# Performance work log

Hardware: AMD Instinct MI355X
Metric: run time of the kernel (lower is better)

Reference implementation:

```python
import jax, jax.numpy as jnp
import numpy as np

SOS_TOKEN = 0


def setup_inputs() -> dict:
    key = jax.random.key(0)
    ks = jax.random.split(key, 16)
    B, S, T, H, V = 64, 64, 32, 512, 32000
    s = 1.0 / np.sqrt(H)
    inp = {
        "encoder_outputs": jax.random.normal(ks[0], (B, S, H), jnp.float32),
        "encoder_hidden": jax.random.normal(ks[1], (1, B, H), jnp.float32),
        "target_tensor": jax.random.randint(ks[2], (B, T), 0, V),
        "emb": jax.random.normal(ks[3], (V, H), jnp.float32),
        "Wa": jax.random.uniform(ks[4], (H, H), jnp.float32, -s, s),
        "ba": jnp.zeros((H,), jnp.float32),
        "Ua": jax.random.uniform(ks[5], (H, H), jnp.float32, -s, s),
        "bu": jnp.zeros((H,), jnp.float32),
        "va": jax.random.uniform(ks[6], (H, 1), jnp.float32, -s, s),
        "bv": jnp.zeros((1,), jnp.float32),
        "w_ih": jax.random.uniform(ks[7], (3 * H, 2 * H), jnp.float32, -s, s),
        "b_ih": jax.random.uniform(ks[8], (3 * H,), jnp.float32, -s, s),
        "w_hh": jax.random.uniform(ks[9], (3 * H, H), jnp.float32, -s, s),
        "b_hh": jax.random.uniform(ks[10], (3 * H,), jnp.float32, -s, s),
        "Wo": jax.random.uniform(ks[11], (V, H), jnp.float32, -s, s),
        "bo": jax.random.uniform(ks[12], (V,), jnp.float32, -s, s),
    }
    return inp


def _gru_cell(x, h, w_ih, b_ih, w_hh, b_hh):
    # x: [B, 2H], h: [B, H] -- PyTorch nn.GRU gate math
    H = h.shape[-1]
    gi = x @ w_ih.T + b_ih            # [B, 3H]
    gh = h @ w_hh.T + b_hh            # [B, 3H]
    i_r, i_z, i_n = gi[:, :H], gi[:, H:2 * H], gi[:, 2 * H:]
    h_r, h_z, h_n = gh[:, :H], gh[:, H:2 * H], gh[:, 2 * H:]
    r = jax.nn.sigmoid(i_r + h_r)
    z = jax.nn.sigmoid(i_z + h_z)
    n = jnp.tanh(i_n + r * h_n)
    return (1.0 - z) * n + z * h


def reference(encoder_outputs, encoder_hidden, target_tensor,
              emb, Wa, ba, Ua, bu, va, bv,
              w_ih, b_ih, w_hh, b_hh, Wo, bo):
    B, S, H = encoder_outputs.shape
    T = target_tensor.shape[1]
    # Teacher forcing: step t input is SOS for t=0 else target[:, t-1]
    sos = jnp.full((B, 1), SOS_TOKEN, dtype=target_tensor.dtype)
    input_ids = jnp.concatenate([sos, target_tensor[:, :-1]], axis=1)  # [B, T]
    embedded = emb[input_ids]  # [B, T, H]  (dropout is identity in eval)

    # Precompute key projection once (invariant across steps)
    Ua_keys = encoder_outputs @ Ua.T + bu  # [B, S, H]

    def step(h, x_emb):
        # Bahdanau additive attention: query = hidden state
        scores = jnp.tanh(h[:, None, :] @ Wa.T + ba + Ua_keys) @ va + bv  # [B, S, 1]
        scores = scores[..., 0]                                           # [B, S]
        attn = jax.nn.softmax(scores, axis=-1)
        context = jnp.einsum('bs,bsh->bh', attn, encoder_outputs)
        x = jnp.concatenate([x_emb, context], axis=-1)                    # [B, 2H]
        h_new = _gru_cell(x, h, w_ih, b_ih, w_hh, b_hh)
        logits = h_new @ Wo.T + bo                                        # [B, V]
        return h_new, (logits, attn)

    h0 = encoder_hidden[0]  # [B, H]
    h_final, (logits_t, attn_t) = jax.lax.scan(step, h0, jnp.swapaxes(embedded, 0, 1))
    logits = jnp.swapaxes(logits_t, 0, 1)        # [B, T, V]
    attentions = jnp.swapaxes(attn_t, 0, 1)      # [B, T, S]
    log_probs = jax.nn.log_softmax(logits, axis=-1)
    decoder_hidden = h_final[None]               # [1, B, H]
    return (log_probs, decoder_hidden, attentions)
```

## Files before the change

### kernel.cpp

```cpp
#include <hip/hip_runtime.h>

typedef unsigned short u16;
typedef __bf16 bf16x8 __attribute__((ext_vector_type(8)));
typedef float f32x4 __attribute__((ext_vector_type(4)));

#define Bsz 64
#define Ssz 64
#define Tsz 32
#define Hsz 512
#define Vsz 32000
#define NCONV 160
#define NTOT 256

static __device__ inline u16 f2bf(float f) {
    union { float f; unsigned u; } v; v.f = f;
    unsigned u = v.u;
    unsigned r = (u + 0x7FFFu + ((u >> 16) & 1u)) >> 16;
    return (u16)r;
}
static __device__ inline float bf2f(u16 v) {
    union { unsigned u; float f; } x; x.u = ((unsigned)v) << 16; return x.f;
}
static __device__ inline float tanh_fast(float x) {
    float e = __expf(2.f * x);
    return 1.f - 2.f / (e + 1.f);
}
static __device__ inline void st_u32(unsigned* p, unsigned v) {
    __hip_atomic_store(p, v, __ATOMIC_RELAXED, __HIP_MEMORY_SCOPE_AGENT);
}
static __device__ inline unsigned ld_u32(const unsigned* p) {
    return __hip_atomic_load(p, __ATOMIC_RELAXED, __HIP_MEMORY_SCOPE_AGENT);
}

#define GLOAD_LDS16(g, l) \
    __builtin_amdgcn_global_load_lds((const __attribute__((address_space(1))) void*)(g), \
                                     (__attribute__((address_space(3))) void*)(l), 16, 0, 0)

__global__ void prep_kernel(const float* __restrict__ enc, const float* __restrict__ Ua,
                            const float* __restrict__ Wa, const float* __restrict__ wih,
                            const float* __restrict__ whh, const float* __restrict__ ehid,
                            const int* __restrict__ target, const float* __restrict__ emb,
                            u16* __restrict__ encbf, u16* __restrict__ Uabf,
                            u16* __restrict__ Wabf, u16* __restrict__ wihbf,
                            u16* __restrict__ whhbf, u16* __restrict__ h0bf,
                            u16* __restrict__ xbuf) {
    const int n0 = 2097152, n1 = 262144, n2 = 262144, n3 = 1572864, n4 = 786432, n5 = 32768;
    const int n6 = Tsz * Bsz * Hsz;
    const int total = n0 + n1 + n2 + n3 + n4 + n5 + n6;
    for (int i = blockIdx.x * blockDim.x + threadIdx.x; i < total; i += gridDim.x * blockDim.x) {
        int j = i;
        if (j < n0) { encbf[j] = f2bf(enc[j]); continue; } j -= n0;
        if (j < n1) { Uabf[j] = f2bf(Ua[j]); continue; } j -= n1;
        if (j < n2) { Wabf[j] = f2bf(Wa[j]); continue; } j -= n2;
        if (j < n3) { wihbf[j] = f2bf(wih[j]); continue; } j -= n3;
        if (j < n4) { whhbf[j] = f2bf(whh[j]); continue; } j -= n4;
        if (j < n5) { h0bf[j] = f2bf(ehid[j]); continue; } j -= n5;
        {
            int t = j / (Bsz * Hsz);
            int rem = j % (Bsz * Hsz);
            int b = rem / Hsz, k = rem % Hsz;
            int id = (t == 0) ? 0 : target[b * Tsz + (t - 1)];
            xbuf[((size_t)t * Bsz + b) * 1024 + k] = f2bf(emb[(size_t)id * Hsz + k]);
        }
    }
}

__global__ __launch_bounds__(256) void gemm_bt(const u16* __restrict__ A, const u16* __restrict__ Bw,
                                               const float* __restrict__ bias, float* __restrict__ out,
                                               int M, int N, int K) {
    __shared__ __align__(16) u16 As[128 * 32];
    __shared__ __align__(16) u16 Bs[128 * 32];
    int m0 = blockIdx.x * 128, n0 = blockIdx.y * 128;
    int tid = threadIdx.x, lane = tid & 63, wid = tid >> 6;
    int wm = wid & 1, wn = wid >> 1;
    f32x4 acc[4][4] = {};
    for (int k0 = 0; k0 < K; k0 += 32) {
        int e0 = wid * 64 + lane;
        int e1 = e0 + 256;
        GLOAD_LDS16(&A[(size_t)(m0 + (e0 >> 2)) * K + k0 + (e0 & 3) * 8], (char*)As + wid * 1024);
        GLOAD_LDS16(&A[(size_t)(m0 + (e1 >> 2)) * K + k0 + (e1 & 3) * 8], (char*)As + 4096 + wid * 1024);
        GLOAD_LDS16(&Bw[(size_t)(n0 + (e0 >> 2)) * K + k0 + (e0 & 3) * 8], (char*)Bs + wid * 1024);
        GLOAD_LDS16(&Bw[(size_t)(n0 + (e1 >> 2)) * K + k0 + (e1 & 3) * 8], (char*)Bs + 4096 + wid * 1024);
        __syncthreads();
        bf16x8 av[4], bvv[4];
        for (int mi = 0; mi < 4; ++mi)
            av[mi] = *(const bf16x8*)&As[(wm * 64 + mi * 16 + (lane & 15)) * 32 + (lane >> 4) * 8];
        for (int ni = 0; ni < 4; ++ni)
            bvv[ni] = *(const bf16x8*)&Bs[(wn * 64 + ni * 16 + (lane & 15)) * 32 + (lane >> 4) * 8];
        for (int mi = 0; mi < 4; ++mi)
            for (int ni = 0; ni < 4; ++ni)
                acc[mi][ni] = __builtin_amdgcn_mfma_f32_16x16x32_bf16(av[mi], bvv[ni], acc[mi][ni], 0, 0, 0);
        __syncthreads();
    }
    for (int mi = 0; mi < 4; ++mi)
        for (int ni = 0; ni < 4; ++ni) {
            int n = n0 + wn * 64 + ni * 16 + (lane & 15);
            float bb = bias[n];
            for (int r = 0; r < 4; ++r) {
                int m = m0 + wm * 64 + mi * 16 + (lane >> 4) * 4 + r;
                out[(size_t)m * N + n] = acc[mi][ni][r] + bb;
            }
        }
}

static __device__ inline void arrive(unsigned* bar, int slot, unsigned val, int tid) {
    asm volatile("s_waitcnt vmcnt(0)" ::: "memory");
    __syncthreads();
    if (tid == 0) st_u32(&bar[slot * 32], val);
}
static __device__ inline void pollflags1(unsigned* bar, int base, int n, unsigned target, int tid) {
    if (tid < n) {
        unsigned* p = &bar[(base + tid) * 32];
        while (ld_u32(p) < target) asm volatile("s_sleep 1");
    }
    __syncthreads();
}

__global__ __launch_bounds__(512, 1) void coop_kernel(
    const float* __restrict__ uak,
    u16* __restrict__ xbuf, u16* __restrict__ Abf,
    const u16* __restrict__ h0bf, const u16* __restrict__ wihbf, const u16* __restrict__ whhbf,
    const u16* __restrict__ Wabf, const float* __restrict__ enc,
    const float* __restrict__ va, const float* __restrict__ bv, const float* __restrict__ ba,
    const float* __restrict__ b_ih, const float* __restrict__ b_hh,
    const float* __restrict__ ehid,
    const float* __restrict__ Wo, u16* __restrict__ Wobf,
    float* __restrict__ out, u16* __restrict__ partials,
    unsigned* __restrict__ bar) {
    __shared__ __align__(16) char lds[149504];
    __shared__ float WhL[512];
    __shared__ float scL[64];
    __shared__ float vaL[512];

    const size_t HID_OFF = (size_t)Bsz * Tsz * Vsz;
    const size_t ATT_OFF = HID_OFF + (size_t)Bsz * Hsz;

    int tid = threadIdx.x, lane = tid & 63, wid = tid >> 6;
    int ln15 = lane & 15, hi = lane >> 4;
    int bx = blockIdx.x;

    unsigned* xbufU = (unsigned*)xbuf;
    unsigned* AbfU = (unsigned*)Abf;
    unsigned* partU = (unsigned*)partials;

    if (bx < 64) {
        int b = bx;
        u16* uakL = (u16*)lds;
        u16* encL = (u16*)(lds + 65536);
        for (int i = tid; i < Ssz * Hsz; i += 512) {
            uakL[i] = f2bf(uak[(size_t)b * Ssz * Hsz + i]);
            encL[i] = f2bf(enc[(size_t)b * Ssz * Hsz + i]);
        }
        vaL[tid] = va[tid];
        float bvv = bv[0];
        float ba_t = ba[tid];
        int halfsel = tid & 1;
        __syncthreads();

        for (int t = 0; t < Tsz; ++t) {
            pollflags1(bar, 64, 32, (unsigned)(t + 1), tid);
            {
                float acc = ba_t;
                const unsigned* pb = partU + (size_t)b * 256 + (tid >> 1);
#pragma unroll
                for (int g = 0; g < 32; ++g) {
                    unsigned pw = ld_u32(pb + (size_t)g * 16384);
                    acc += bf2f((u16)(halfsel ? (pw >> 16) : (pw & 0xffff)));
                }
                WhL[tid] = acc;
            }
            __syncthreads();
            for (int si = 0; si < 8; ++si) {
                int s = wid * 8 + si;
                float a = 0.f;
#pragma unroll
                for (int ji = 0; ji < 8; ++ji) {
                    int j = lane + ji * 64;
                    float x = WhL[j] + bf2f(uakL[s * 512 + j]);
                    a += tanh_fast(x) * vaL[j];
                }
                for (int off = 32; off; off >>= 1) a += __shfl_down(a, off);
                if (lane == 0) scL[s] = a + bvv;
            }
            __syncthreads();
            if (wid == 0) {
                float x = scL[lane];
                float mx = x;
                for (int off = 32; off; off >>= 1) mx = fmaxf(mx, __shfl_xor(mx, off));
                float e = __expf(x - mx);
                float sm = e;
                for (int off = 32; off; off >>= 1) sm += __shfl_xor(sm, off);
                float at = e / sm;
                scL[lane] = at;
                out[ATT_OFF + ((size_t)b * Tsz + t) * Ssz + lane] = at;
            }
            __syncthreads();
            float c = 0.f;
            for (int s = 0; s < Ssz; ++s)
                c += scL[s] * bf2f(encL[s * 512 + tid]);
            unsigned me = (unsigned)f2bf(c);
            unsigned other = __shfl_xor(me, 1);
            if ((tid & 1) == 0)
                st_u32(&xbufU[((size_t)t * Bsz + b) * 512 + 256 + (tid >> 1)], me | (other << 16));
            arrive(bar, bx, (unsigned)(t + 1), tid);
        }
    } else if (bx < 96) {
        int g = bx - 64, jbase = g * 16;
        u16* hsl = (u16*)(lds + 147456);
        for (int i = tid; i < 6144; i += 512) {
            int row = i >> 7, c16 = i & 127;
            int Rg = (row >> 4) * 512 + jbase + (row & 15);
            uint4 v = *(const uint4*)&wihbf[(size_t)Rg * 1024 + c16 * 8];
            *(uint4*)(lds + row * 2048 + ((c16 * 16) ^ ((row & 7) << 4))) = v;
        }
        for (int i = tid; i < 3072; i += 512) {
            int row = i >> 6, c16 = i & 63;
            int Rg = (row >> 4) * 512 + jbase + (row & 15);
            uint4 v = *(const uint4*)&whhbf[(size_t)Rg * 512 + c16 * 8];
            *(uint4*)(lds + 98304 + row * 1024 + ((c16 * 16) ^ ((row & 7) << 4))) = v;
        }
        const char* wih_l = lds;
        const char* whh_l = lds + 98304;
        int j = jbase + ln15;
        float bir = b_ih[j] + b_hh[j];
        float biz = b_ih[512 + j] + b_hh[512 + j];
        float bin = b_ih[1024 + j];
        float bhn = b_hh[1024 + j];
        float hp0 = 0.f, hp1 = 0.f, hp2 = 0.f, hp3 = 0.f;
        if (wid < 4) {
            int m = wid;
            hp0 = ehid[(size_t)(m * 16 + hi * 4 + 0) * Hsz + j];
            hp1 = ehid[(size_t)(m * 16 + hi * 4 + 1) * Hsz + j];
            hp2 = ehid[(size_t)(m * 16 + hi * 4 + 2) * Hsz + j];
            hp3 = ehid[(size_t)(m * 16 + hi * 4 + 3) * Hsz + j];
        }
        int swz = (ln15 & 7) << 4;
        bf16x8 zfr = {};
        bf16x8 wfrag[4];
#pragma unroll
        for (int i = 0; i < 4; ++i) {
            int jp = (wid * 4 + i) * 16 + ln15;
            wfrag[i] = (hi < 2) ? *(const bf16x8*)&Wabf[(size_t)jp * 512 + jbase + hi * 8] : zfr;
        }
        for (int i = tid; i < 1024; i += 512)
            hsl[i] = h0bf[(size_t)(i >> 4) * 512 + jbase + (i & 15)];
        __syncthreads();
#pragma unroll
        for (int mt = 0; mt < 4; ++mt) {
            bf16x8 af = (hi < 2) ? *(const bf16x8*)&hsl[(mt * 16 + ln15) * 16 + hi * 8] : zfr;
#pragma unroll
            for (int i = 0; i < 4; ++i) {
                f32x4 pacc = {};
                pacc = __builtin_amdgcn_mfma_f32_16x16x32_bf16(af, wfrag[i], pacc, 0, 0, 0);
                int n0 = (wid * 4 + i) * 16;
#pragma unroll
                for (int r = 0; r < 4; ++r) {
                    int b = mt * 16 + hi * 4 + r;
                    unsigned me = (unsigned)f2bf(pacc[r]);
                    unsigned other = __shfl_xor(me, 1);
                    if ((ln15 & 1) == 0)
                        st_u32(&partU[((size_t)g * 64 + b) * 256 + ((n0 + ln15) >> 1)], me | (other << 16));
                }
            }
        }
        arrive(bar, bx, 1u, tid);

        for (int t = 0; t < Tsz; ++t) {
            const u16* hbt = t ? (Abf + (size_t)(t - 1) * Bsz * Hsz) : h0bf;
            f32x4 ar = {}, az = {}, ain = {}, ahn = {};
            if (wid < 4) {
                int m = wid;
#pragma unroll 8
                for (int k0 = 0; k0 < 16; ++k0) {
                    bf16x8 a = *(const bf16x8*)&xbuf[((size_t)t * Bsz + m * 16 + ln15) * 1024 + k0 * 32 + hi * 8];
                    int byteIn = k0 * 64 + hi * 16;
                    bf16x8 b0 = *(const bf16x8*)(wih_l + (0 + ln15) * 2048 + (byteIn ^ swz));
                    bf16x8 b1 = *(const bf16x8*)(wih_l + (16 + ln15) * 2048 + (byteIn ^ swz));
                    bf16x8 b2 = *(const bf16x8*)(wih_l + (32 + ln15) * 2048 + (byteIn ^ swz));
                    ar = __builtin_amdgcn_mfma_f32_16x16x32_bf16(a, b0, ar, 0, 0, 0);
                    az = __builtin_amdgcn_mfma_f32_16x16x32_bf16(a, b1, az, 0, 0, 0);
                    ain = __builtin_amdgcn_mfma_f32_16x16x32_bf16(a, b2, ain, 0, 0, 0);
                }
            }
            pollflags1(bar, 64, 32, (unsigned)(t + 1), tid);
            if (wid < 4) {
                int m = wid;
#pragma unroll 8
                for (int k0 = 0; k0 < 16; ++k0) {
                    bf16x8 a = *(const bf16x8*)&hbt[(size_t)(m * 16 + ln15) * 512 + k0 * 32 + hi * 8];
                    int byteIn = k0 * 64 + hi * 16;
                    bf16x8 b0 = *(const bf16x8*)(whh_l + (0 + ln15) * 1024 + (byteIn ^ swz));
                    bf16x8 b1 = *(const bf16x8*)(whh_l + (16 + ln15) * 1024 + (byteIn ^ swz));
                    bf16x8 b2 = *(const bf16x8*)(whh_l + (32 + ln15) * 1024 + (byteIn ^ swz));
                    ar = __builtin_amdgcn_mfma_f32_16x16x32_bf16(a, b0, ar, 0, 0, 0);
                    az = __builtin_amdgcn_mfma_f32_16x16x32_bf16(a, b1, az, 0, 0, 0);
                    ahn = __builtin_amdgcn_mfma_f32_16x16x32_bf16(a, b2, ahn, 0, 0, 0);
                }
                unsigned* p = &bar[(wid * 16 + ln15) * 32];
                while (ld_u32(p) < (unsigned)(t + 1)) asm volatile("s_sleep 1");
#pragma unroll 8
                for (int k0 = 16; k0 < 32; ++k0) {
                    bf16x8 a = *(const bf16x8*)&xbuf[((size_t)t * Bsz + m * 16 + ln15) * 1024 + k0 * 32 + hi * 8];
                    int byteIn = k0 * 64 + hi * 16;
                    bf16x8 b0 = *(const bf16x8*)(wih_l + (0 + ln15) * 2048 + (byteIn ^ swz));
                    bf16x8 b1 = *(const bf16x8*)(wih_l + (16 + ln15) * 2048 + (byteIn ^ swz));
                    bf16x8 b2 = *(const bf16x8*)(wih_l + (32 + ln15) * 2048 + (byteIn ^ swz));
                    ar = __builtin_amdgcn_mfma_f32_16x16x32_bf16(a, b0, ar, 0, 0, 0);
                    az = __builtin_amdgcn_mfma_f32_16x16x32_bf16(a, b1, az, 0, 0, 0);
                    ain = __builtin_amdgcn_mfma_f32_16x16x32_bf16(a, b2, ain, 0, 0, 0);
                }
                float hpv[4] = {hp0, hp1, hp2, hp3};
#pragma unroll
                for (int r = 0; r < 4; ++r) {
                    int b = m * 16 + hi * 4 + r;
                    float rg = 1.f / (1.f + __expf(-(ar[r] + bir)));
                    float zg = 1.f / (1.f + __expf(-(az[r] + biz)));
                    float ng = tanh_fast(ain[r] + bin + rg * (ahn[r] + bhn));
                    float hv = (1.f - zg) * ng + zg * hpv[r];
                    hpv[r] = hv;
                    u16 hb = f2bf(hv);
                    unsigned me = (unsigned)hb;
                    unsigned other = __shfl_xor(me, 1);
                    if ((ln15 & 1) == 0)
                        st_u32(&AbfU[((size_t)t * Bsz + b) * 256 + (j >> 1)], me | (other << 16));
                    hsl[b * 16 + ln15] = hb;
                    if (t == Tsz - 1) out[HID_OFF + (size_t)b * 512 + j] = hv;
                }
                hp0 = hpv[0]; hp1 = hpv[1]; hp2 = hpv[2]; hp3 = hpv[3];
            }
            __syncthreads();
#pragma unroll
            for (int mt = 0; mt < 4; ++mt) {
                bf16x8 af = (hi < 2) ? *(const bf16x8*)&hsl[(mt * 16 + ln15) * 16 + hi * 8] : zfr;
#pragma unroll
                for (int i = 0; i < 4; ++i) {
                    f32x4 pacc = {};
                    pacc = __builtin_amdgcn_mfma_f32_16x16x32_bf16(af, wfrag[i], pacc, 0, 0, 0);
                    int n0 = (wid * 4 + i) * 16;
#pragma unroll
                    for (int r = 0; r < 4; ++r) {
                        int b = mt * 16 + hi * 4 + r;
                        unsigned me = (unsigned)f2bf(pacc[r]);
                        unsigned other = __shfl_xor(me, 1);
                        if ((ln15 & 1) == 0)
                            st_u32(&partU[((size_t)g * 64 + b) * 256 + ((n0 + ln15) >> 1)], me | (other << 16));
                    }
                }
            }
            arrive(bar, bx, (unsigned)(t + 2), tid);
        }
    } else {
        const float4* W4 = (const float4*)Wo;
        for (int i = (bx - 96) * 512 + tid; i < (Vsz * Hsz) / 4; i += NCONV * 512) {
            float4 v = W4[i];
            ushort4 o;
            o.x = f2bf(v.x); o.y = f2bf(v.y); o.z = f2bf(v.z); o.w = f2bf(v.w);
            *(ushort4*)&Wobf[(size_t)i * 4] = o;
        }
    }
}

template <int BF16OUT>
__global__ __launch_bounds__(512) void gemm_logits(const u16* __restrict__ Abf, const u16* __restrict__ Wobf,
                                                   const float* __restrict__ bo, float* __restrict__ out,
                                                   u16* __restrict__ scr, float* __restrict__ sumexp) {
    __shared__ __align__(16) char lds[49152];
    char* As0 = lds;
    char* Bs0 = lds + 8192;
    char* As1 = lds + 24576;
    char* Bs1 = lds + 32768;
    int tid = threadIdx.x, lane = tid & 63, wid = tid >> 6;
    int ln15 = lane & 15, hi = lane >> 4;
    int wm = wid & 1, wn = wid >> 1;
    int job = blockIdx.x;
    int m0 = (job / 125) * 128, n0 = (job % 125) * 256;
    f32x4 acc[4][4] = {};
    {
        int e0 = wid * 64 + lane, r = e0 >> 2, c8 = (e0 & 3) * 8;
        GLOAD_LDS16(&Abf[(size_t)(m0 + r) * 512 + c8], As0 + wid * 1024);
        GLOAD_LDS16(&Wobf[(size_t)(n0 + r) * 512 + c8], Bs0 + wid * 1024);
        GLOAD_LDS16(&Wobf[(size_t)(n0 + 128 + r) * 512 + c8], Bs0 + 8192 + wid * 1024);
    }
#pragma unroll 2
    for (int ks = 0; ks < 16; ++ks) {
        const u16* As = (const u16*)((ks & 1) ? As1 : As0);
        const u16* Bs = (const u16*)((ks & 1) ? Bs1 : Bs0);
        if (ks < 15) {
            char* Asn = (ks & 1) ? As0 : As1;
            char* Bsn = (ks & 1) ? Bs0 : Bs1;
            int e0 = wid * 64 + lane, r = e0 >> 2, c8 = (e0 & 3) * 8;
            int k0 = (ks + 1) * 32;
            GLOAD_LDS16(&Abf[(size_t)(m0 + r) * 512 + k0 + c8], Asn + wid * 1024);
            GLOAD_LDS16(&Wobf[(size_t)(n0 + r) * 512 + k0 + c8], Bsn + wid * 1024);
            GLOAD_LDS16(&Wobf[(size_t)(n0 + 128 + r) * 512 + k0 + c8], Bsn + 8192 + wid * 1024);
            asm volatile("s_waitcnt vmcnt(3)" ::: "memory");
        } else {
            asm volatile("s_waitcnt vmcnt(0)" ::: "memory");
        }
        __builtin_amdgcn_s_barrier();
        bf16x8 av[4], bvv[4];
        for (int mi = 0; mi < 4; ++mi)
            av[mi] = *(const bf16x8*)&As[(wm * 64 + mi * 16 + ln15) * 32 + hi * 8];
        for (int ni = 0; ni < 4; ++ni)
            bvv[ni] = *(const bf16x8*)&Bs[(wn * 64 + ni * 16 + ln15) * 32 + hi * 8];
        for (int mi = 0; mi < 4; ++mi)
            for (int ni = 0; ni < 4; ++ni)
                acc[mi][ni] = __builtin_amdgcn_mfma_f32_16x16x32_bf16(av[mi], bvv[ni], acc[mi][ni], 0, 0, 0);
        asm volatile("s_waitcnt lgkmcnt(0)" ::: "memory");
        __builtin_amdgcn_s_barrier();
    }
    float* eps = (float*)lds;
    float bb[4];
#pragma unroll
    for (int ni = 0; ni < 4; ++ni) bb[ni] = bo[n0 + wn * 64 + ni * 16 + ln15];
    for (int mi = 0; mi < 4; ++mi) {
        __syncthreads();
#pragma unroll
        for (int ni = 0; ni < 4; ++ni)
#pragma unroll
            for (int r = 0; r < 4; ++r)
                eps[(wm * 16 + hi * 4 + r) * 256 + wn * 64 + ni * 16 + ln15] = acc[mi][ni][r] + bb[ni];
        __syncthreads();
#pragma unroll
        for (int k = 0; k < 4; ++k) {
            int idx = k * 512 + tid;
            int l = idx >> 6, c4 = idx & 63;
            int m = m0 + (l >> 4) * 64 + mi * 16 + (l & 15);
            int t = m >> 6, b = m & 63;
            float4 v = *(float4*)&eps[l * 256 + c4 * 4];
            if (BF16OUT) {
                ushort4 o;
                o.x = f2bf(v.x); o.y = f2bf(v.y); o.z = f2bf(v.z); o.w = f2bf(v.w);
                *(ushort4*)&scr[((size_t)(b * Tsz + t)) * Vsz + n0 + c4 * 4] = o;
            } else {
                *(float4*)&out[((size_t)(b * Tsz + t)) * Vsz + n0 + c4 * 4] = v;
            }
            float e = __expf(v.x) + __expf(v.y) + __expf(v.z) + __expf(v.w);
            for (int off = 32; off; off >>= 1) e += __shfl_down(e, off);
            if (lane == 0) atomicAdd(&sumexp[(m & 63) * Tsz + (m >> 6)], e);
        }
    }
}

__global__ void sub_kernel(float* __restrict__ out, const float* __restrict__ sumexp) {
    const int total4 = (Bsz * Tsz * Vsz) / 4;
    float4* o4 = (float4*)out;
    for (int i = blockIdx.x * blockDim.x + threadIdx.x; i < total4; i += gridDim.x * blockDim.x) {
        float l = __logf(sumexp[i / (Vsz / 4)]);
        float4 v = o4[i];
        v.x -= l; v.y -= l; v.z -= l; v.w -= l;
        o4[i] = v;
    }
}

__global__ void sub_bf16_kernel(const u16* __restrict__ scr, const float* __restrict__ sumexp,
                                float* __restrict__ out) {
    const int total8 = (Bsz * Tsz * Vsz) / 8;
    for (int i = blockIdx.x * blockDim.x + threadIdx.x; i < total8; i += gridDim.x * blockDim.x) {
        float l = __logf(sumexp[i / (Vsz / 8)]);
        uint4 v = *(const uint4*)&scr[(size_t)i * 8];
        float4 a, b;
        a.x = bf2f((u16)v.x) - l;        a.y = bf2f((u16)(v.x >> 16)) - l;
        a.z = bf2f((u16)v.y) - l;        a.w = bf2f((u16)(v.y >> 16)) - l;
        b.x = bf2f((u16)v.z) - l;        b.y = bf2f((u16)(v.z >> 16)) - l;
        b.z = bf2f((u16)v.w) - l;        b.w = bf2f((u16)(v.w >> 16)) - l;
        *(float4*)&out[(size_t)i * 8] = a;
        *(float4*)&out[(size_t)i * 8 + 4] = b;
    }
}

extern "C" void kernel_launch(void* const* d_in, const int* in_sizes, int n_in,
                              void* d_out, int out_size, void* d_ws, size_t ws_size,
                              hipStream_t stream) {
    const float* enc   = (const float*)d_in[0];
    const float* ehid  = (const float*)d_in[1];
    const int*   target= (const int*)d_in[2];
    const float* emb   = (const float*)d_in[3];
    const float* Wa    = (const float*)d_in[4];
    const float* ba    = (const float*)d_in[5];
    const float* Ua    = (const float*)d_in[6];
    const float* bu    = (const float*)d_in[7];
    const float* va    = (const float*)d_in[8];
    const float* bv    = (const float*)d_in[9];
    const float* w_ih  = (const float*)d_in[10];
    const float* b_ih  = (const float*)d_in[11];
    const float* w_hh  = (const float*)d_in[12];
    const float* b_hh  = (const float*)d_in[13];
    const float* Wo    = (const float*)d_in[14];
    const float* bo    = (const float*)d_in[15];
    float* out = (float*)d_out;

    char* w = (char*)d_ws;
    float* uak    = (float*)w; w += (size_t)4096 * 512 * 4;
    float* sumexp = (float*)w; w += 8192;
    unsigned* bar = (unsigned*)w; w += 128 * 128;
    u16* xbuf     = (u16*)w;   w += (size_t)Tsz * Bsz * 1024 * 2;
    u16* Abf      = (u16*)w;   w += (size_t)Tsz * Bsz * Hsz * 2;
    u16* h0bf     = (u16*)w;   w += (size_t)Bsz * Hsz * 2;
    u16* partials = (u16*)w;   w += (size_t)32 * Bsz * Hsz * 2;
    u16* Wabf     = (u16*)w;   w += (size_t)Hsz * Hsz * 2;
    u16* encbf    = (u16*)w;   w += (size_t)4096 * 512 * 2;
    u16* Uabf     = (u16*)w;   w += (size_t)Hsz * Hsz * 2;
    u16* wihbf    = (u16*)w;   w += (size_t)1536 * 1024 * 2;
    u16* whhbf    = (u16*)w;   w += (size_t)1536 * 512 * 2;
    u16* Wobf     = (u16*)w;   w += (size_t)Vsz * 512 * 2;
    u16* scrbf    = (u16*)w;   w += (size_t)Bsz * Tsz * Vsz * 2;
    const int use_bf16 = (ws_size >= (size_t)(w - (char*)d_ws));

    prep_kernel<<<2048, 256, 0, stream>>>(enc, Ua, Wa, w_ih, w_hh, ehid, target, emb,
                                          encbf, Uabf, Wabf, wihbf, whhbf, h0bf, xbuf);

    gemm_bt<<<dim3(32, 4), 256, 0, stream>>>(encbf, Uabf, bu, uak, 4096, 512, 512);

    hipMemsetAsync(bar, 0, 128 * 128, stream);
    hipMemsetAsync(sumexp, 0, 2048 * 4, stream);

    coop_kernel<<<NTOT, 512, 0, stream>>>(uak, xbuf, Abf, h0bf, wihbf, whhbf,
                                          Wabf, enc, va, bv, ba, b_ih, b_hh,
                                          ehid, Wo, Wobf, out, partials, bar);

    if (use_bf16) {
        gemm_logits<1><<<2000, 512, 0, stream>>>(Abf, Wobf, bo, out, scrbf, sumexp);
        sub_bf16_kernel<<<4096, 256, 0, stream>>>(scrbf, sumexp, out);
    } else {
        gemm_logits<0><<<2000, 512, 0, stream>>>(Abf, Wobf, bo, out, scrbf, sumexp);
        sub_kernel<<<2048, 256, 0, stream>>>(out, sumexp);
    }
}
```

Measured before the change: 823.0 us.

## Replace shared flag barriers with per-pair mailboxes and buffer attention output in LDS

Each producer block now writes its progress flag into a separate mailbox slot for every consumer, replacing the single flag per block that all consumers polled. Each consumer polls only its own contiguous mailboxes, which is meant to cut contention and cache-line ping-pong on the shared flags in the per-step cross-block handshake. Attention weights are also kept in LDS across all steps and written to global memory once at the end, removing small global stores from the serial loop. The cost is more flag stores per arrival and a larger barrier region to memset.

Measured after the change: 819.3 us. Within noise of the previous version (-0.4%).

```diff
diff --git a/kernel.cpp b/kernel.cpp
--- a/kernel.cpp
+++ b/kernel.cpp
@@ -11,6 +11,11 @@
 #define Vsz 32000
 #define NCONV 160
 #define NTOT 256
+
+#define MAIL_BG 0
+#define MAIL_GB 2048
+#define MAIL_GG 4096
+#define NMAIL 5120
 
 static __device__ inline u16 f2bf(float f) {
     union { float f; unsigned u; } v; v.f = f;
@@ -103,19 +108,6 @@
         }
 }
 
-static __device__ inline void arrive(unsigned* bar, int slot, unsigned val, int tid) {
-    asm volatile("s_waitcnt vmcnt(0)" ::: "memory");
-    __syncthreads();
-    if (tid == 0) st_u32(&bar[slot * 32], val);
-}
-static __device__ inline void pollflags1(unsigned* bar, int base, int n, unsigned target, int tid) {
-    if (tid < n) {
-        unsigned* p = &bar[(base + tid) * 32];
-        while (ld_u32(p) < target) asm volatile("s_sleep 1");
-    }
-    __syncthreads();
-}
-
 __global__ __launch_bounds__(512, 1) void coop_kernel(
     const float* __restrict__ uak,
     u16* __restrict__ xbuf, u16* __restrict__ Abf,
@@ -147,6 +139,7 @@
         int b = bx;
         u16* uakL = (u16*)lds;
         u16* encL = (u16*)(lds + 65536);
+        float* attL = (float*)(lds + 131072);
         for (int i = tid; i < Ssz * Hsz; i += 512) {
             uakL[i] = f2bf(uak[(size_t)b * Ssz * Hsz + i]);
             encL[i] = f2bf(enc[(size_t)b * Ssz * Hsz + i]);
@@ -158,7 +151,11 @@
         __syncthreads();
 
         for (int t = 0; t < Tsz; ++t) {
-            pollflags1(bar, 64, 32, (unsigned)(t + 1), tid);
+            if (tid < 32) {
+                unsigned* p = &bar[(MAIL_GB + b * 32 + tid) * 32];
+                while (ld_u32(p) < (unsigned)(t + 1)) asm volatile("s_sleep 1");
+            }
+            __syncthreads();
             {
                 float acc = ba_t;
                 const unsigned* pb = partU + (size_t)b * 256 + (tid >> 1);
@@ -192,7 +189,7 @@
                 for (int off = 32; off; off >>= 1) sm += __shfl_xor(sm, off);
                 float at = e / sm;
                 scL[lane] = at;
-                out[ATT_OFF + ((size_t)b * Tsz + t) * Ssz + lane] = at;
+                attL[t * 64 + lane] = at;
             }
             __syncthreads();
             float c = 0.f;
@@ -202,8 +199,13 @@
             unsigned other = __shfl_xor(me, 1);
             if ((tid & 1) == 0)
                 st_u32(&xbufU[((size_t)t * Bsz + b) * 512 + 256 + (tid >> 1)], me | (other << 16));
-            arrive(bar, bx, (unsigned)(t + 1), tid);
-        }
+            asm volatile("s_waitcnt vmcnt(0)" ::: "memory");
+            __syncthreads();
+            if (tid < 32) st_u32(&bar[(MAIL_BG + tid * 64 + b) * 32], (unsigned)(t + 1));
+        }
+        __syncthreads();
+        for (int i = tid; i < Tsz * Ssz; i += 512)
+            out[ATT_OFF + (size_t)b * (Tsz * Ssz) + i] = attL[i];
     } else if (bx < 96) {
         int g = bx - 64, jbase = g * 16;
         u16* hsl = (u16*)(lds + 147456);
@@ -263,7 +265,10 @@
                 }
             }
         }
-        arrive(bar, bx, 1u, tid);
+        asm volatile("s_waitcnt vmcnt(0)" ::: "memory");
+        __syncthreads();
+        if (tid < 64) st_u32(&bar[(MAIL_GB + tid * 32 + g) * 32], 1u);
+        else if (tid < 96) st_u32(&bar[(MAIL_GG + (tid - 64) * 32 + g) * 32], 1u);
 
         for (int t = 0; t < Tsz; ++t) {
             const u16* hbt = t ? (Abf + (size_t)(t - 1) * Bsz * Hsz) : h0bf;
@@ -282,7 +287,11 @@
                     ain = __builtin_amdgcn_mfma_f32_16x16x32_bf16(a, b2, ain, 0, 0, 0);
                 }
             }
-            pollflags1(bar, 64, 32, (unsigned)(t + 1), tid);
+            if (tid < 32) {
+                unsigned* p = &bar[(MAIL_GG + g * 32 + tid) * 32];
+                while (ld_u32(p) < (unsigned)(t + 1)) asm volatile("s_sleep 1");
+            }
+            __syncthreads();
             if (wid < 4) {
                 int m = wid;
 #pragma unroll 8
@@ -296,7 +305,7 @@
                     az = __builtin_amdgcn_mfma_f32_16x16x32_bf16(a, b1, az, 0, 0, 0);
                     ahn = __builtin_amdgcn_mfma_f32_16x16x32_bf16(a, b2, ahn, 0, 0, 0);
                 }
-                unsigned* p = &bar[(wid * 16 + ln15) * 32];
+                unsigned* p = &bar[(MAIL_BG + g * 64 + wid * 16 + ln15) * 32];
                 while (ld_u32(p) < (unsigned)(t + 1)) asm volatile("s_sleep 1");
 #pragma unroll 8
                 for (int k0 = 16; k0 < 32; ++k0) {
@@ -347,7 +356,10 @@
                     }
                 }
             }
-            arrive(bar, bx, (unsigned)(t + 2), tid);
+            asm volatile("s_waitcnt vmcnt(0)" ::: "memory");
+            __syncthreads();
+            if (tid < 64) st_u32(&bar[(MAIL_GB + tid * 32 + g) * 32], (unsigned)(t + 2));
+            else if (tid < 96) st_u32(&bar[(MAIL_GG + (tid - 64) * 32 + g) * 32], (unsigned)(t + 2));
         }
     } else {
         const float4* W4 = (const float4*)Wo;
@@ -493,7 +505,7 @@
     char* w = (char*)d_ws;
     float* uak    = (float*)w; w += (size_t)4096 * 512 * 4;
     float* sumexp = (float*)w; w += 8192;
-    unsigned* bar = (unsigned*)w; w += 128 * 128;
+    unsigned* bar = (unsigned*)w; w += (size_t)NMAIL * 128;
     u16* xbuf     = (u16*)w;   w += (size_t)Tsz * Bsz * 1024 * 2;
     u16* Abf      = (u16*)w;   w += (size_t)Tsz * Bsz * Hsz * 2;
     u16* h0bf     = (u16*)w;   w += (size_t)Bsz * Hsz * 2;
@@ -512,7 +524,7 @@
 
     gemm_bt<<<dim3(32, 4), 256, 0, stream>>>(encbf, Uabf, bu, uak, 4096, 512, 512);
 
-    hipMemsetAsync(bar, 0, 128 * 128, stream);
+    hipMemsetAsync(bar, 0, (size_t)NMAIL * 128, stream);
     hipMemsetAsync(sumexp, 0, 2048 * 4, stream);
 
     coop_kernel<<<NTOT, 512, 0, stream>>>(uak, xbuf, Abf, h0bf, wihbf, whhbf,
```
